# Performance work log

Hardware: AMD Instinct MI355X
Metric: run time of the kernel (lower is better)

The kernel has to match this reference:

```python
import jax, jax.numpy as jnp
import numpy as np

NUM_BITS = 8
NUM_STEPS = 2 ** NUM_BITS - 2  # 254, clamp range -127..127


def _roundpass(x):
    # straight-through round: forward=round, backward=identity
    return x + jax.lax.stop_gradient(jnp.round(x) - x)


def _quantize(x, alpha, always_pos=False):
    # Quantizer.quantize with use_ste=True, is_on=True
    alpha = jax.nn.relu(alpha)  # relu(alpha_baseline + alpha_delta)
    stepsize = 2.0 * alpha / NUM_STEPS
    off = alpha if always_pos else 0.0
    scaled = (x - off) / stepsize
    clamped = jnp.clip(_roundpass(scaled), -(NUM_STEPS // 2), NUM_STEPS // 2)
    return clamped * stepsize + off


def setup_inputs() -> dict:
    key = jax.random.key(0)
    k1, k2 = jax.random.split(key)
    x = jax.random.normal(k1, (32, 64, 56, 56), dtype=jnp.float32)
    w = jax.random.normal(k2, (128, 64, 3, 3), dtype=jnp.float32) * 0.05
    alpha_x = jnp.ones((1,), dtype=jnp.float32)
    alpha_w = jnp.ones((1,), dtype=jnp.float32)
    return {"x": x, "w": w, "alpha_x": alpha_x, "alpha_w": alpha_w}


def reference(x, w, alpha_x, alpha_w):
    # quantize activations and weights (8-bit symmetric, STE round)
    qx = _quantize(x, alpha_x[0], always_pos=False)
    qw = _quantize(w, alpha_w[0], always_pos=False)
    # im2col lowering + tiled_mm accumulation over K-tiles is exactly a
    # stride-1 conv with padding (1,1); tile padding in M/N/K contributes
    # only zeros and is sliced off, so plain conv is the faithful math.
    out = jax.lax.conv_general_dilated(
        qx, qw,
        window_strides=(1, 1),
        padding=((1, 1), (1, 1)),
        dimension_numbers=("NCHW", "OIHW", "NCHW"),
    )  # [32, 128, 56, 56]
    return out
```

## Files before the change

kernel.cpp:

```cpp
#include <hip/hip_runtime.h>
#include <hip/hip_bf16.h>

typedef int   v4i __attribute__((ext_vector_type(4)));
typedef float v4f __attribute__((ext_vector_type(4)));

#define HWSZ 3136
#define IMW  56
#define PADW 58
#define PHW  3364
#define CIN  64
#define COUT 128
#define ROWB 3712

__device__ __forceinline__ float step_size(float a) {
    a = a > 0.f ? a : 0.f;
    return 2.0f * a / 254.0f;
}

__device__ __forceinline__ int quant1(float x, float s) {
    float v = rintf(x / s);
    v = fminf(127.f, fmaxf(-127.f, v));
    return (int)v;
}

__device__ __forceinline__ unsigned int pack4(int a, int b, int c, int d) {
    return (unsigned int)(a & 255) | ((unsigned int)(b & 255) << 8) |
           ((unsigned int)(c & 255) << 16) | ((unsigned int)(d & 255) << 24);
}

__device__ __forceinline__ void gload_lds16(const signed char* g, signed char* l) {
    __builtin_amdgcn_global_load_lds(
        (const __attribute__((address_space(1))) void*)g,
        (__attribute__((address_space(3))) void*)l, 16, 0, 0);
}

__global__ __launch_bounds__(256) void quant_kernel(const float* __restrict__ x,
                                                    const float* __restrict__ w,
                                                    const float* __restrict__ alpha_x,
                                                    const float* __restrict__ alpha_w,
                                                    signed char* __restrict__ cx,
                                                    signed char* __restrict__ wt) {
    int t = threadIdx.x;
    int b = blockIdx.x;
    if (b >= 1568) {
        if (b >= 1856) {
            int q = (b - 1856) * 256 + t;
            int n = q / 912;
            int r = q % 912;
            int px = r >> 2, seg = r & 3;
            int ph, pw;
            if (px < 58)       { ph = 0;  pw = px; }
            else if (px < 116) { ph = 57; pw = px - 58; }
            else { int k = px - 116; ph = 1 + (k >> 1); pw = (k & 1) * 57; }
            v4i z = {0, 0, 0, 0};
            *(v4i*)(cx + ((size_t)n * PHW + ph * PADW + pw) * 64 + seg * 16) = z;
            return;
        }
        float s = step_size(alpha_w[0]);
        int j = (b - 1568) * 256 + t;
        int tap = j / 8192;
        int r   = j % 8192;
        int o   = r >> 6;
        int c   = r & 63;
        float v = w[((size_t)o * 64 + c) * 9 + tap];
        wt[j] = (signed char)quant1(v, s);
        return;
    }

    __shared__ unsigned int tile32[64 * 17];
    float s = step_size(alpha_x[0]);
    int n   = b / 49;
    int hw0 = (b % 49) * 64;
    int g   = t & 15;
    int cq  = t >> 4;
    int p   = t >> 2;
    int seg = t & 3;

    const float* xb = x + ((size_t)n * CIN + cq * 4) * HWSZ + hw0 + g * 4;
    v4f f0 = *(const v4f*)(xb);
    v4f f1 = *(const v4f*)(xb + HWSZ);
    v4f f2 = *(const v4f*)(xb + 2 * HWSZ);
    v4f f3 = *(const v4f*)(xb + 3 * HWSZ);
#pragma unroll
    for (int j = 0; j < 4; ++j) {
        unsigned int u = pack4(quant1(f0[j], s), quant1(f1[j], s),
                               quant1(f2[j], s), quant1(f3[j], s));
        tile32[(g * 4 + j) * 17 + cq] = u;
    }
    __syncthreads();
    int base = p * 17 + seg * 4;
    v4i val;
    val[0] = (int)tile32[base + 0];
    val[1] = (int)tile32[base + 1];
    val[2] = (int)tile32[base + 2];
    val[3] = (int)tile32[base + 3];
    int hw = hw0 + p;
    int h = hw / IMW, wq = hw % IMW;
    *(v4i*)(cx + ((size_t)n * PHW + (h + 1) * PADW + (wq + 1)) * 64 + seg * 16) = val;
}

__global__ __launch_bounds__(256, 3) void conv_kernel(const signed char* __restrict__ cx,
                                                      const signed char* __restrict__ wt,
                                                      const float* __restrict__ ax,
                                                      const float* __restrict__ aw,
                                                      float* __restrict__ out) {
    __shared__ __attribute__((aligned(16))) signed char as_[29184];
    float scale = step_size(ax[0]) * step_size(aw[0]);
    int tid  = threadIdx.x;
    int lane = tid & 63;
    int wid  = tid >> 6;
    int row  = lane & 15;
    int kg   = lane >> 4;

    int bid = blockIdx.x;
    int swz = (bid & 7) * 112 + (bid >> 3);
    int n   = swz / 28;
    int tl  = swz % 28;
    int hw0 = tl * 112;
    int h0  = tl * 2;
    int us  = h0 - 1;

    const signed char* wsrc = cx + ((size_t)n * PHW + (size_t)h0 * PADW) * 64;
#pragma unroll
    for (int r = 0; r < 4; ++r) {
        int slotbase = r * 256 + wid * 64;
        gload_lds16(wsrc + (size_t)(slotbase + lane) * 16, as_ + slotbase * 16);
    }

    int obase = wid * 32;
    const signed char* wb = wt + (obase + row) * 64 + kg * 16;
    v4i breg[9][2];
#pragma unroll
    for (int tap = 0; tap < 9; ++tap)
#pragma unroll
        for (int ot = 0; ot < 2; ++ot)
            breg[tap][ot] = *(const v4i*)(wb + tap * (COUT * 64) + ot * (16 * 64));

    int lbase[7];
#pragma unroll
    for (int pt = 0; pt < 7; ++pt) {
        int hwp = hw0 + pt * 16 + row;
        int hh  = hwp / IMW, ww = hwp % IMW;
        lbase[pt] = (hh - us) * ROWB + (ww + 1) * 64 + kg * 16;
    }

    asm volatile("s_waitcnt vmcnt(0)" ::: "memory");
    __syncthreads();
#pragma unroll
    for (int tap = 0; tap < 9; ++tap)
#pragma unroll
        for (int ot = 0; ot < 2; ++ot)
            asm volatile("" :: "v"(breg[tap][ot]));

    v4i acc[7][2] = {};
#pragma unroll
    for (int tap = 0; tap < 9; ++tap) {
        int doff = (tap / 3 - 1) * ROWB + (tap % 3 - 1) * 64;
        v4i a[7];
#pragma unroll
        for (int pt = 0; pt < 7; ++pt)
            a[pt] = *(const v4i*)(as_ + lbase[pt] + doff);
#pragma unroll
        for (int pt = 0; pt < 7; ++pt)
#pragma unroll
            for (int ot = 0; ot < 2; ++ot)
                acc[pt][ot] = __builtin_amdgcn_mfma_i32_16x16x64_i8(a[pt], breg[tap][ot], acc[pt][ot], 0, 0, 0);
    }

    __syncthreads();
    signed char* scrw = as_ + wid * 7296;
    float* obb = out + ((size_t)n * COUT) * HWSZ + hw0;
    int og = lane >> 5;
    (void)og;

#pragma unroll
    for (int rr = 0; rr < 2; ++rr) {
#pragma unroll
        for (int pt = 0; pt < 7; ++pt) {
            v4f v;
            v[0] = scale * (float)acc[pt][rr][0];
            v[1] = scale * (float)acc[pt][rr][1];
            v[2] = scale * (float)acc[pt][rr][2];
            v[3] = scale * (float)acc[pt][rr][3];
            *(v4f*)(scrw + row * 456 + pt * 64 + kg * 16) = v;
        }
        if (lane < 56) {
            int g2 = lane / 28;
            int c  = lane - g2 * 28;
#pragma unroll
            for (int j = 0; j < 8; ++j) {
                int ol = j * 2 + g2;
                v4f v = *(const v4f*)(scrw + ol * 456 + c * 16);
                int o = obase + rr * 16 + ol;
                *(v4f*)(obb + (size_t)o * HWSZ + c * 4) = v;
            }
        }
        __builtin_amdgcn_s_waitcnt(0);
    }
}

extern "C" void kernel_launch(void* const* d_in, const int* in_sizes, int n_in,
                              void* d_out, int out_size, void* d_ws, size_t ws_size,
                              hipStream_t stream) {
    const float* x  = (const float*)d_in[0];
    const float* w  = (const float*)d_in[1];
    const float* ax = (const float*)d_in[2];
    const float* aw = (const float*)d_in[3];
    float* out = (float*)d_out;

    signed char* cx = (signed char*)d_ws;
    signed char* wt = cx + 6889472;

    quant_kernel<<<1970, 256, 0, stream>>>(x, w, ax, aw, cx, wt);
    conv_kernel<<<896, 256, 0, stream>>>(cx, wt, ax, aw, out);
}
```

Measured before the change: 34.39 us.

## Retile conv blocks to 8 image rows per block with output-channel quarters

Each conv block now covers 8 output rows (448 pixels) for one quarter of the output channels, with all four waves sharing the same channel slice instead of splitting channels across waves. The LDS halo load grows to 10 rows, so the halo overhead per pixel drops. The epilogue is rewritten to stage a full 16x448 float tile in LDS, with all 64 lanes writing longer contiguous output rows. The trade-off is more LDS per block (40 KB), which may lower occupancy, and each input tile is now reloaded by four blocks.

Result: faster. 32.10 us (-6.7%).

```diff
diff --git a/kernel.cpp b/kernel.cpp
--- a/kernel.cpp
+++ b/kernel.cpp
@@ -11,6 +11,7 @@
 #define CIN  64
 #define COUT 128
 #define ROWB 3712
+#define SROW 1824
 
 __device__ __forceinline__ float step_size(float a) {
     a = a > 0.f ? a : 0.f;
@@ -104,7 +105,7 @@
                                                       const float* __restrict__ ax,
                                                       const float* __restrict__ aw,
                                                       float* __restrict__ out) {
-    __shared__ __attribute__((aligned(16))) signed char as_[29184];
+    __shared__ __attribute__((aligned(16))) signed char as_[40960];
     float scale = step_size(ax[0]) * step_size(aw[0]);
     int tid  = threadIdx.x;
     int lane = tid & 63;
@@ -112,23 +113,25 @@
     int row  = lane & 15;
     int kg   = lane >> 4;
 
-    int bid = blockIdx.x;
-    int swz = (bid & 7) * 112 + (bid >> 3);
-    int n   = swz / 28;
-    int tl  = swz % 28;
-    int hw0 = tl * 112;
-    int h0  = tl * 2;
-    int us  = h0 - 1;
+    int bid  = blockIdx.x;
+    int swz  = (bid & 7) * 112 + (bid >> 3);
+    int tile = swz >> 2;
+    int oq   = swz & 3;
+    int n    = tile / 7;
+    int rg   = tile % 7;
+    int h0   = rg * 8;
+    int px0  = rg * 448;
 
     const signed char* wsrc = cx + ((size_t)n * PHW + (size_t)h0 * PADW) * 64;
 #pragma unroll
-    for (int r = 0; r < 4; ++r) {
+    for (int r = 0; r < 10; ++r) {
         int slotbase = r * 256 + wid * 64;
-        gload_lds16(wsrc + (size_t)(slotbase + lane) * 16, as_ + slotbase * 16);
-    }
-
-    int obase = wid * 32;
-    const signed char* wb = wt + (obase + row) * 64 + kg * 16;
+        if (slotbase + lane < 2320)
+            gload_lds16(wsrc + (size_t)(slotbase + lane) * 16, as_ + slotbase * 16);
+    }
+
+    int ob = oq * 32;
+    const signed char* wb = wt + (ob + row) * 64 + kg * 16;
     v4i breg[9][2];
 #pragma unroll
     for (int tap = 0; tap < 9; ++tap)
@@ -139,9 +142,9 @@
     int lbase[7];
 #pragma unroll
     for (int pt = 0; pt < 7; ++pt) {
-        int hwp = hw0 + pt * 16 + row;
-        int hh  = hwp / IMW, ww = hwp % IMW;
-        lbase[pt] = (hh - us) * ROWB + (ww + 1) * 64 + kg * 16;
+        int px = px0 + wid * 112 + pt * 16 + row;
+        int hh = px / IMW, ww = px % IMW;
+        lbase[pt] = (hh - h0 + 1) * ROWB + (ww + 1) * 64 + kg * 16;
     }
 
     asm volatile("s_waitcnt vmcnt(0)" ::: "memory");
@@ -167,35 +170,33 @@
                 acc[pt][ot] = __builtin_amdgcn_mfma_i32_16x16x64_i8(a[pt], breg[tap][ot], acc[pt][ot], 0, 0, 0);
     }
 
-    __syncthreads();
-    signed char* scrw = as_ + wid * 7296;
-    float* obb = out + ((size_t)n * COUT) * HWSZ + hw0;
-    int og = lane >> 5;
-    (void)og;
-
+    float* obb = out + ((size_t)n * COUT) * HWSZ + px0;
 #pragma unroll
     for (int rr = 0; rr < 2; ++rr) {
+        __syncthreads();
 #pragma unroll
         for (int pt = 0; pt < 7; ++pt) {
+            int g = wid * 28 + pt * 4 + kg;
             v4f v;
             v[0] = scale * (float)acc[pt][rr][0];
             v[1] = scale * (float)acc[pt][rr][1];
             v[2] = scale * (float)acc[pt][rr][2];
             v[3] = scale * (float)acc[pt][rr][3];
-            *(v4f*)(scrw + row * 456 + pt * 64 + kg * 16) = v;
+            *(v4f*)(as_ + row * SROW + g * 16) = v;
         }
-        if (lane < 56) {
-            int g2 = lane / 28;
-            int c  = lane - g2 * 28;
-#pragma unroll
-            for (int j = 0; j < 8; ++j) {
-                int ol = j * 2 + g2;
-                v4f v = *(const v4f*)(scrw + ol * 456 + c * 16);
-                int o = obase + rr * 16 + ol;
-                *(v4f*)(obb + (size_t)o * HWSZ + c * 4) = v;
+        __syncthreads();
+#pragma unroll
+        for (int r2 = 0; r2 < 4; ++r2) {
+            int r4 = wid * 4 + r2;
+            int o  = ob + rr * 16 + r4;
+            float* orow = obb + (size_t)o * HWSZ;
+            v4f v0 = *(const v4f*)(as_ + r4 * SROW + lane * 16);
+            *(v4f*)(orow + lane * 4) = v0;
+            if (lane < 48) {
+                v4f v1 = *(const v4f*)(as_ + r4 * SROW + (64 + lane) * 16);
+                *(v4f*)(orow + (64 + lane) * 4) = v1;
             }
         }
-        __builtin_amdgcn_s_waitcnt(0);
     }
 }
 
```
